# Optimization experiments

Measured on AMD Instinct MI355X. Metric: run time of the kernel, lower is better.

Reference implementation:

```python
import jax, jax.numpy as jnp
import numpy as np

NUM_HEADS = 8
EMBED_DIM = 512
EXPAND = 3
RPE_DIM = 512
RPE_LAYERS = 3
B, N = 4, 2048
D1 = (EXPAND * EMBED_DIM) // NUM_HEADS * NUM_HEADS  # 1536
HEAD_DIM = D1 // NUM_HEADS  # 192


def srms(x):
    # SimpleRMSNorm: x / (||x||_2 * d^{-1/2} + eps)
    d = x.shape[-1]
    rms = jnp.linalg.norm(x, axis=-1, keepdims=True) * (d ** -0.5)
    return x / (rms + 1e-8)


def rpe_net(idx, Wp, bp, Wl, bl, Wr, br):
    # idx: (m, 1) relative positions -> (m, h*head_dim)
    h = idx @ Wp.T + bp
    for i in range(Wl.shape[0]):  # fixed small layer count
        h = jax.nn.relu(srms(h)) @ Wl[i].T + bl[i]
    return jax.nn.relu(srms(h)) @ Wr.T + br


def setup_inputs() -> dict:
    key = jax.random.key(0)
    ks = jax.random.split(key, 12)
    s = 0.02
    return {
        "x": jax.random.normal(ks[0], (B, N, EMBED_DIM), jnp.float32),
        "Wu": jax.random.normal(ks[1], (D1, EMBED_DIM), jnp.float32) * s,
        "bu": jnp.zeros((D1,), jnp.float32),
        "Wv": jax.random.normal(ks[2], (D1, EMBED_DIM), jnp.float32) * s,
        "bv": jnp.zeros((D1,), jnp.float32),
        "Wo": jax.random.normal(ks[3], (EMBED_DIM, D1), jnp.float32) * s,
        "bo": jnp.zeros((EMBED_DIM,), jnp.float32),
        "Wp": jax.random.normal(ks[4], (RPE_DIM, 1), jnp.float32) * s,
        "bp": jax.random.normal(ks[5], (RPE_DIM,), jnp.float32) * s,
        "Wl": jax.random.normal(ks[6], (RPE_LAYERS, RPE_DIM, RPE_DIM), jnp.float32) * s,
        "bl": jax.random.normal(ks[7], (RPE_LAYERS, RPE_DIM), jnp.float32) * s,
        "Wr": jax.random.normal(ks[8], (NUM_HEADS * HEAD_DIM, RPE_DIM), jnp.float32) * s,
        "br": jax.random.normal(ks[9], (NUM_HEADS * HEAD_DIM,), jnp.float32) * s,
    }


def reference(x, Wu, bu, Wv, bv, Wo, bo, Wp, bp, Wl, bl, Wr, br):
    b, n, e = x.shape
    d1 = Wu.shape[0]
    hd = d1 // NUM_HEADS
    u = jax.nn.silu(x @ Wu.T + bu)                       # (b, n, d1)
    v = jax.nn.silu(x @ Wv.T + bv)                       # (b, n, d1)
    v = v.reshape(b, n, NUM_HEADS, hd).transpose(0, 2, 1, 3)  # (b, h, n, d)
    # Tno non-causal, par_type=1: indices [0, 1..n-1, 0, -(n-1)..-1]
    pos = jnp.arange(1, n, dtype=x.dtype)
    zero = jnp.zeros((1,), x.dtype)
    idx = jnp.concatenate([zero, pos, zero, -pos[::-1]])[:, None]  # (2n, 1)
    a = rpe_net(idx, Wp, bp, Wl, bl, Wr, br)             # (2n, h*d)
    a = a.reshape(2 * n, NUM_HEADS, hd).transpose(1, 0, 2)  # (h, 2n, d)
    m = 2 * n
    # circular conv of length 2n along sequence, truncate to n
    y = jnp.fft.rfft(v, m, axis=2) * jnp.fft.rfft(a, m, axis=1)[None]
    out = jnp.fft.irfft(y, m, axis=2)[:, :, :n, :]       # (b, h, n, d)
    out = out.transpose(0, 2, 1, 3).reshape(b, n, d1)    # (b, n, d1)
    return (u * out) @ Wo.T + bo
```

## Files before the change

kernel.cpp:

```cpp
#include <hip/hip_runtime.h>

#define N_SEQ 2048
#define M_FFT 4096
#define D1    1536
#define NH    8
#define HD    192
#define ED    512

typedef __bf16 bf16;
typedef __bf16 bf16x4 __attribute__((ext_vector_type(4)));
typedef __bf16 bf16x8 __attribute__((ext_vector_type(8)));
typedef float  floatx4 __attribute__((ext_vector_type(4)));
typedef float  cx __attribute__((ext_vector_type(2)));

enum { MODE_PLAIN = 0, MODE_SILU_UV = 1, MODE_AT = 3, MODE_RPE = 4 };

__device__ __forceinline__ void gload16(const void* g, void* l) {
    __builtin_amdgcn_global_load_lds(
        (const __attribute__((address_space(1))) void*)g,
        (__attribute__((address_space(3))) void*)l, 16, 0, 0);
}

template<int MODE, typename OutT>
__global__ __launch_bounds__(256) void gemm_bf16(
    const bf16* __restrict__ A, const bf16* __restrict__ Bw,
    const float* __restrict__ bias, const float* __restrict__ bias2,
    OutT* __restrict__ C, OutT* __restrict__ C2,
    int M, int Nc, int K,
    const float* __restrict__ scale_in, float* __restrict__ sumsq_out)
{
    __shared__ __align__(16) bf16 As[2][128 * 32];
    __shared__ __align__(16) bf16 Bs[2][128 * 32];

    const int tid  = threadIdx.x;
    const int row0 = blockIdx.y * 128;
    const int col0 = blockIdx.x * 128;
    const int wid  = tid >> 6;
    const int lane = tid & 63;
    const int lm   = lane & 15;
    const int lk   = lane >> 4;
    const int wm   = wid >> 1;
    const int wn   = wid & 1;
    const int ldrow  = tid >> 2;
    const int ldcol8 = (tid & 3) * 8;

    floatx4 acc[4][4] = {};

    const bf16* Ag = A  + ((size_t)(row0 + ldrow)) * K + ldcol8;
    const bf16* Bg = Bw + ((size_t)(col0 + ldrow)) * K + ldcol8;
    const int woff = (wid * 16) * 32;

    auto stage = [&](int k0, int buf) {
        gload16(Ag + k0, &As[buf][woff]);
        gload16(Ag + (size_t)64 * K + k0, &As[buf][woff + 64 * 32]);
        gload16(Bg + k0, &Bs[buf][woff]);
        gload16(Bg + (size_t)64 * K + k0, &Bs[buf][woff + 64 * 32]);
    };
    auto compute = [&](int buf) {
        bf16x8 af[4], bfr[4];
        #pragma unroll
        for (int mi = 0; mi < 4; ++mi)
            af[mi] = *(const bf16x8*)&As[buf][(wm * 64 + mi * 16 + lm) * 32 + lk * 8];
        #pragma unroll
        for (int nj = 0; nj < 4; ++nj)
            bfr[nj] = *(const bf16x8*)&Bs[buf][(wn * 64 + nj * 16 + lm) * 32 + lk * 8];
        #pragma unroll
        for (int mi = 0; mi < 4; ++mi)
            #pragma unroll
            for (int nj = 0; nj < 4; ++nj)
                acc[mi][nj] = __builtin_amdgcn_mfma_f32_16x16x32_bf16(
                    af[mi], bfr[nj], acc[mi][nj], 0, 0, 0);
    };

    const int nt = K >> 5;
    stage(0, 0);
    __syncthreads();
    for (int t = 0; t < nt; t += 2) {
        stage((t + 1) << 5, 1);
        compute(0);
        __syncthreads();
        if (t + 2 < nt) stage((t + 2) << 5, 0);
        compute(1);
        __syncthreads();
    }

    const float* bs = bias;
    OutT* dst = C;
    int cadj = 0;
    if (MODE == MODE_SILU_UV && col0 >= D1) { bs = bias2; dst = C2; cadj = D1; }

    float bcol[4];
    #pragma unroll
    for (int nj = 0; nj < 4; ++nj)
        bcol[nj] = bs[col0 - cadj + wn * 64 + nj * 16 + lm];

    if (MODE == MODE_RPE) {
        #pragma unroll
        for (int mi = 0; mi < 4; ++mi) {
            #pragma unroll
            for (int r = 0; r < 4; ++r) {
                const int row = row0 + wm * 64 + mi * 16 + lk * 4 + r;
                float sc = 1.0f;
                if (scale_in)
                    sc = 1.0f / (sqrtf(scale_in[row]) * 0.04419417382415922f + 1e-8f);
                float ssq = 0.0f;
                #pragma unroll
                for (int nj = 0; nj < 4; ++nj) {
                    const int col = col0 + wn * 64 + nj * 16 + lm;
                    float val = acc[mi][nj][r] * sc + bcol[nj];
                    ssq += val * val;
                    ((bf16*)C)[(size_t)row * Nc + col] = (bf16)fmaxf(val, 0.0f);
                }
                ssq += __shfl_xor(ssq, 1, 64);
                ssq += __shfl_xor(ssq, 2, 64);
                ssq += __shfl_xor(ssq, 4, 64);
                ssq += __shfl_xor(ssq, 8, 64);
                if (lm == 0) atomicAdd(&sumsq_out[row], ssq);
            }
        }
        return;
    }

    #pragma unroll
    for (int mi = 0; mi < 4; ++mi) {
        const int rbase = row0 + wm * 64 + mi * 16 + lk * 4;
        float sc[4];
        #pragma unroll
        for (int r = 0; r < 4; ++r) {
            sc[r] = 1.0f;
            if (MODE == MODE_AT && scale_in)
                sc[r] = 1.0f / (sqrtf(scale_in[rbase + r]) * 0.04419417382415922f + 1e-8f);
        }
        #pragma unroll
        for (int nj = 0; nj < 4; ++nj) {
            const int col = col0 - cadj + wn * 64 + nj * 16 + lm;
            float vals[4];
            #pragma unroll
            for (int r = 0; r < 4; ++r) {
                float val = acc[mi][nj][r] * sc[r] + bcol[nj];
                if (MODE == MODE_SILU_UV)
                    val = val / (1.0f + __expf(-val));
                vals[r] = val;
            }
            if (MODE == MODE_SILU_UV) {
                int b = rbase >> 11, s = rbase & 2047;
                bf16x4 o;
                #pragma unroll
                for (int r = 0; r < 4; ++r) o[r] = (bf16)vals[r];
                *(bf16x4*)&((bf16*)dst)[((size_t)(b * D1 + col)) * N_SEQ + s] = o;
            } else if (MODE == MODE_AT) {
                float4 o = make_float4(vals[0], vals[1], vals[2], vals[3]);
                *(float4*)&((float*)C)[(size_t)col * M + rbase] = o;
            } else {
                #pragma unroll
                for (int r = 0; r < 4; ++r)
                    C[(size_t)(rbase + r) * Nc + col] = (OutT)vals[r];
            }
        }
    }
}

__global__ __launch_bounds__(256) void f2b_all_kernel(
    const float* __restrict__ x,  const float* __restrict__ s0,
    const float* __restrict__ s1, const float* __restrict__ s2,
    const float* __restrict__ s3, const float* __restrict__ s4,
    const float* __restrict__ Wp, const float* __restrict__ bp,
    bf16* __restrict__ x_bf, bf16* __restrict__ w_bf,
    float* __restrict__ sumsq, bf16* __restrict__ g0,
    float* __restrict__ twd)
{
    const int bid = blockIdx.x;
    const int tid = threadIdx.x;
    __shared__ float red[4];

    if (bid < 7936) {
        const float* src;
        bf16* dst;
        size_t off;
        if (bid < 4096) {
            src = x; dst = x_bf; off = (size_t)bid * 1024;
        } else {
            int t = bid - 4096;
            int seg = t / 768;
            src = seg == 0 ? s0 : seg == 1 ? s1 : seg == 2 ? s2
                : seg == 3 ? s3 : s4;
            dst = w_bf + (size_t)seg * 786432;
            off = (size_t)(t % 768) * 1024;
        }
        size_t i = off + (size_t)tid * 4;
        float4 f = *(const float4*)(src + i);
        union { bf16 h[4]; short4 s; } u4;
        u4.h[0] = (bf16)f.x; u4.h[1] = (bf16)f.y;
        u4.h[2] = (bf16)f.z; u4.h[3] = (bf16)f.w;
        *(short4*)(dst + i) = u4.s;
    } else if (bid < 7948) {
        size_t i = (size_t)(bid - 7936) * 1024 + (size_t)tid * 4;
        *(float4*)(sumsq + i) = make_float4(0.f, 0.f, 0.f, 0.f);
    } else if (bid < 12044) {
        const int j = bid - 7948;
        float idxv = (j < N_SEQ) ? (float)j
                                 : (j == N_SEQ ? 0.0f : (float)(j - 2 * N_SEQ));
        float h1 = idxv * Wp[tid] + bp[tid];
        float h2 = idxv * Wp[tid + 256] + bp[tid + 256];
        float ss = h1 * h1 + h2 * h2;
        #pragma unroll
        for (int off = 32; off > 0; off >>= 1) ss += __shfl_down(ss, off, 64);
        if ((tid & 63) == 0) red[tid >> 6] = ss;
        __syncthreads();
        float tot = red[0] + red[1] + red[2] + red[3];
        float scale = 1.0f / (sqrtf(tot) * 0.04419417382415922f + 1e-8f);
        g0[(size_t)j * ED + tid]       = (bf16)fmaxf(h1 * scale, 0.0f);
        g0[(size_t)j * ED + tid + 256] = (bf16)fmaxf(h2 * scale, 0.0f);
    } else {
        const int idx = (bid - 12044) * 256 + tid;
        const int j = idx >> 4, tau = idx & 15;
        float sA, cA;
        __sincosf(-6.283185307179586f * (float)(j * tau) * (1.0f / 4096.0f),
                  &sA, &cA);
        cx w; w.x = cA; w.y = sA;
        ((cx*)twd)[idx] = w;
    }
}

#define FFT_LDS_SZ 4381

__device__ __forceinline__ int fpad(int i) { return i + (i >> 4) + 2 * (i >> 8); }

__device__ __forceinline__ cx mkcx(float a, float b) { cx r; r.x = a; r.y = b; return r; }
__device__ __forceinline__ cx cmul(cx a, cx b) {
    cx br = mkcx(-b.y, b.x);
    return a.xx * b + a.yy * br;
}
__device__ __forceinline__ cx cmul_cj(cx a, cx b) {
    cx bc = mkcx(b.x, -b.y);
    cx br = mkcx(b.y, b.x);
    return a.xx * bc + a.yy * br;
}
__device__ __forceinline__ cx cneg_i(cx a) { return mkcx(a.y, -a.x); }
__device__ __forceinline__ cx cpos_i(cx a) { return mkcx(-a.y, a.x); }
__host__ __device__ constexpr int brev4(int t) {
    return ((t & 1) << 3) | ((t & 2) << 1) | ((t & 4) >> 1) | ((t & 8) >> 3);
}

#define CC1 0.9238795325112867f
#define SS1 0.3826834323650898f
#define RR2 0.7071067811865476f

template<bool HZ>
__device__ __forceinline__ void fft16_dif_r4(cx x[16]) {
    const cx W1 = mkcx( CC1, -SS1);
    const cx W2 = mkcx( RR2, -RR2);
    const cx W3 = mkcx( SS1, -CC1);
    const cx W6 = mkcx(-RR2, -RR2);
    const cx W9 = mkcx(-CC1,  SS1);
    #pragma unroll
    for (int n = 0; n < 4; ++n) {
        cx A, B, C, D;
        if (HZ) { A = x[n]; C = x[n]; B = x[n + 4]; D = x[n + 4]; }
        else {
            A = x[n] + x[n + 8];      C = x[n] - x[n + 8];
            B = x[n + 4] + x[n + 12]; D = x[n + 4] - x[n + 12];
        }
        cx s = A - B;
        cx nid = cneg_i(D);
        cx m = C + nid;
        cx p = C - nid;
        x[n] = A + B;
        if (n == 0)      { x[4] = s;            x[8]  = m;           x[12] = p; }
        else if (n == 1) { x[5] = cmul(s, W2);  x[9]  = cmul(m, W1); x[13] = cmul(p, W3); }
        else if (n == 2) { x[6] = cneg_i(s);    x[10] = cmul(m, W2); x[14] = cmul(p, W6); }
        else             { x[7] = cmul(s, W6);  x[11] = cmul(m, W3); x[15] = cmul(p, W9); }
    }
    #pragma unroll
    for (int q = 0; q < 16; q += 4) {
        cx a = x[q], b = x[q + 1], c = x[q + 2], d = x[q + 3];
        cx a1 = a + c, c1 = a - c;
        cx b1 = b + d, d1 = cneg_i(b - d);
        x[q]     = a1 + b1;
        x[q + 1] = a1 - b1;
        x[q + 2] = c1 + d1;
        x[q + 3] = c1 - d1;
    }
}

template<bool HALF_OUT>
__device__ __forceinline__ void fft16_dit_inv_r4(cx x[16]) {
    const cx V1 = mkcx( CC1, SS1);
    const cx V2 = mkcx( RR2, RR2);
    const cx V3 = mkcx( SS1, CC1);
    const cx V6 = mkcx(-RR2, RR2);
    #pragma unroll
    for (int q = 0; q < 16; q += 4) {
        cx a = x[q], b = x[q + 1], c = x[q + 2], d = x[q + 3];
        cx a1 = a + b, b1 = a - b;
        cx c1 = c + d, d1 = c - d;
        cx t = cpos_i(d1);
        x[q]     = a1 + c1;
        x[q + 2] = a1 - c1;
        x[q + 1] = b1 + t;
        x[q + 3] = b1 - t;
    }
    #pragma unroll
    for (int n = 0; n < 4; ++n) {
        cx t1, t2;
        if (n == 0)      { t1 = x[4];             t2 = x[12]; }
        else if (n == 1) { t1 = cmul(x[5],  V2);  t2 = cmul(x[13], V2); }
        else if (n == 2) { t1 = cpos_i(x[6]);     t2 = cpos_i(x[14]); }
        else             { t1 = cmul(x[7],  V6);  t2 = cmul(x[15], V6); }
        cx P = x[n] + t1, Q = x[n] - t1;
        cx R = x[n + 8] + t2, S = x[n + 8] - t2;
        cx t, u;
        if (n == 0)      { t = R;            u = S; }
        else if (n == 1) { t = cmul(R, V1);  u = cmul(S, V1); }
        else if (n == 2) { t = cmul(R, V2);  u = cmul(S, V2); }
        else             { t = cmul(R, V3);  u = cmul(S, V3); }
        cx iu = cpos_i(u);
        x[n]     = P + t;
        x[n + 4] = Q + iu;
        if (!HALF_OUT) {
            x[n + 8]  = P - t;
            x[n + 12] = Q - iu;
        }
    }
}

template<bool CONJ>
__device__ __forceinline__ void apply_tw(cx v[16], const cx tw[16]) {
    #pragma unroll
    for (int tau = 1; tau < 16; ++tau) {
        const int q = brev4(tau);
        v[q] = CONJ ? cmul_cj(v[q], tw[tau]) : cmul(v[q], tw[tau]);
    }
}

template<bool CONJ>
__device__ __forceinline__ void apply_tw_lds(cx v[16], const cx* twrow) {
    #pragma unroll
    for (int tau = 1; tau < 16; ++tau) {
        cx w = twrow[tau * 16];
        const int q = brev4(tau);
        v[q] = CONJ ? cmul_cj(v[q], w) : cmul(v[q], w);
    }
}

__device__ __forceinline__ void fwd_s1_store_hz(
    const cx vin[8], const cx tw[16], cx* d, int tid)
{
    cx x[16];
    #pragma unroll
    for (int t = 0; t < 8; ++t) x[t] = vin[t];
    fft16_dif_r4<true>(x);
    apply_tw<false>(x, tw);
    cx* base = d + fpad(tid);
    #pragma unroll
    for (int p = 0; p < 16; ++p) base[274 * p] = x[p];
}

__device__ __forceinline__ void fwd_s2(cx* d, int tid, const cx* tw2lds)
{
    cx v[16];
    cx* base = d + fpad(((tid >> 4) << 8) + (tid & 15));
    #pragma unroll
    for (int t = 0; t < 16; ++t) v[t] = base[17 * t];
    fft16_dif_r4<false>(v);
    apply_tw_lds<false>(v, tw2lds + (tid & 15));
    #pragma unroll
    for (int p = 0; p < 16; ++p) base[17 * p] = v[p];
}

__device__ __forceinline__ void fwd_s3(cx* d, int tid)
{
    cx v[16];
    cx* base = d + fpad(tid << 4);
    #pragma unroll
    for (int t = 0; t < 16; ++t) v[t] = base[t];
    fft16_dif_r4<false>(v);
    #pragma unroll
    for (int p = 0; p < 16; ++p) base[p] = v[p];
}

__device__ __forceinline__ void inv_s2(cx* d, int tid, const cx* tw2lds)
{
    cx v[16];
    cx* base = d + fpad(((tid >> 4) << 8) + (tid & 15));
    #pragma unroll
    for (int p = 0; p < 16; ++p) v[p] = base[17 * p];
    apply_tw_lds<true>(v, tw2lds + (tid & 15));
    fft16_dit_inv_r4<false>(v);
    #pragma unroll
    for (int t = 0; t < 16; ++t) base[17 * t] = v[t];
}

__device__ __forceinline__ void inv_s3_half(cx* d, int tid, const cx tw[16])
{
    cx v[16];
    cx* base = d + fpad(tid);
    #pragma unroll
    for (int p = 0; p < 16; ++p) v[p] = base[274 * p];
    apply_tw<true>(v, tw);
    fft16_dit_inv_r4<true>(v);
    #pragma unroll
    for (int t = 0; t < 8; ++t) base[274 * t] = v[t];
}

__device__ __forceinline__ void pointwise_read(
    const cx* d, int tid, const float4 a0pf[8], const float4 a1pf[8],
    cx v[16])
{
    auto pf = [](const float4* p, int i) -> cx {
        return (i & 1) ? mkcx(p[i >> 1].z, p[i >> 1].w)
                       : mkcx(p[i >> 1].x, p[i >> 1].y);
    };
    const int pbase = tid << 4;
    if (tid == 0) {
        #pragma unroll
        for (int i = 0; i < 16; ++i) {
            const int p2 = (i < 2) ? i : (i ^ ((1 << (31 - __clz(i))) - 1));
            cx Zk = d[fpad(i)];
            cx Zm = d[fpad(p2)];
            cx cjZm = mkcx(Zm.x, -Zm.y);
            cx V0 = Zk + cjZm;
            cx V1 = cneg_i(Zk - cjZm);
            v[i] = cmul(V0, pf(a0pf, i)) + cpos_i(cmul(V1, pf(a1pf, i)));
        }
    } else {
        const int mask = (1 << (31 - __clz(pbase))) - 1;
        const cx* zb  = d + fpad(pbase);
        const cx* zb2 = d + fpad((pbase ^ mask) - 15);
        #pragma unroll
        for (int i = 0; i < 16; ++i) {
            cx Zk = zb[i];
            cx Zm = zb2[15 - i];
            cx cjZm = mkcx(Zm.x, -Zm.y);
            cx V0 = Zk + cjZm;
            cx V1 = cneg_i(Zk - cjZm);
            v[i] = cmul(V0, pf(a0pf, i)) + cpos_i(cmul(V1, pf(a1pf, i)));
        }
    }
}

template<bool HALF_ZERO>
__device__ __forceinline__ void fft4096_fwd_core(
    cx* d, int tid, const cx tw[16], const cx* tw2lds, cx v[16])
{
    {
        fft16_dif_r4<HALF_ZERO>(v);
        apply_tw<false>(v, tw);
        cx* base = d + fpad(tid);
        #pragma unroll
        for (int p = 0; p < 16; ++p) base[274 * p] = v[p];
    }
    __syncthreads();
    fwd_s2(d, tid, tw2lds);
    __syncthreads();
    fwd_s3(d, tid);
    __syncthreads();
}

__global__ __launch_bounds__(256, 4) void fft_a_kernel(
    const float* a_t, cx* __restrict__ A0s, cx* A1s,
    const cx* __restrict__ Twd)
{
    __shared__ cx data[FFT_LDS_SZ];
    __shared__ cx tw2lds[256];
    const int tid = threadIdx.x;
    const int r = blockIdx.x;

    cx tw[16];
    {
        const cx* Tr1 = Twd + (tid << 4);
        #pragma unroll
        for (int t = 1; t < 16; ++t) tw[t] = Tr1[t];
        tw2lds[(tid >> 4) * 16 + (tid & 15)] = Twd[(tid & 15) * 256 + (tid >> 4)];
    }

    const float* r0 = a_t + (size_t)(2 * r) * M_FFT;
    const float* r1 = r0 + M_FFT;
    cx v[16];
    #pragma unroll
    for (int t = 0; t < 16; ++t)
        v[t] = mkcx(r0[tid + 256 * t], r1[tid + 256 * t]);

    fft4096_fwd_core<false>(data, tid, tw, tw2lds, v);

    const float c = 0.25f / 4096.0f;
    cx* A0row = A0s + (size_t)r * 4096;
    cx* A1row = A1s + (size_t)r * 4096;
    if (tid == 0) {
        #pragma unroll
        for (int i = 0; i < 16; ++i) {
            const int p2 = (i < 2) ? i : (i ^ ((1 << (31 - __clz(i))) - 1));
            cx Wk = data[fpad(i)];
            cx Wm = data[fpad(p2)];
            cx cjWm = mkcx(Wm.x, -Wm.y);
            A0row[i] = c * (Wk + cjWm);
            A1row[i] = c * cneg_i(Wk - cjWm);
        }
    } else {
        const int base = tid << 4;
        const int mask = (1 << (31 - __clz(base))) - 1;
        const cx* zb  = data + fpad(base);
        const cx* zb2 = data + fpad((base ^ mask) - 15);
        #pragma unroll
        for (int i = 0; i < 16; ++i) {
            cx Wk = zb[i];
            cx Wm = zb2[15 - i];
            cx cjWm = mkcx(Wm.x, -Wm.y);
            A0row[base + i] = c * (Wk + cjWm);
            A1row[base + i] = c * cneg_i(Wk - cjWm);
        }
    }
}

__global__ __launch_bounds__(256, 2) void fft_conv_kernel(
    const bf16* __restrict__ v_t, const cx* __restrict__ A0s,
    const cx* __restrict__ A1s, const bf16* __restrict__ u_t,
    bf16* __restrict__ gated_t, const cx* __restrict__ Twd)
{
    __shared__ cx data[2][FFT_LDS_SZ];
    __shared__ cx tw2lds[256];
    const int tid = threadIdx.x;
    const int bx = blockIdx.x;
    const int xcd  = bx & 7;
    const int slot = bx >> 3;
    const int bp   = slot & 1;
    const int r    = (slot >> 1) * 8 + xcd;
    const int ch   = 2 * r;
    const int b0   = 2 * bp;
    const int b1   = 2 * bp + 1;

    cx tw[16];
    {
        const cx* Tr1 = Twd + (tid << 4);
        #pragma unroll
        for (int t = 1; t < 16; ++t) tw[t] = Tr1[t];
        tw2lds[(tid >> 4) * 16 + (tid & 15)] = Twd[(tid & 15) * 256 + (tid >> 4)];
    }

    const bf16* z00 = v_t + ((size_t)(b0 * D1 + ch)) * N_SEQ;
    const bf16* z01 = z00 + N_SEQ;
    const bf16* z10 = v_t + ((size_t)(b1 * D1 + ch)) * N_SEQ;
    const bf16* z11 = z10 + N_SEQ;
    {
        cx w0[8], w1[8];
        #pragma unroll
        for (int t = 0; t < 8; ++t)
            w0[t] = mkcx((float)z00[tid + 256 * t], (float)z01[tid + 256 * t]);
        #pragma unroll
        for (int t = 0; t < 8; ++t)
            w1[t] = mkcx((float)z10[tid + 256 * t], (float)z11[tid + 256 * t]);
        fwd_s1_store_hz(w0, tw, data[0], tid);
        fwd_s1_store_hz(w1, tw, data[1], tid);
    }
    __syncthreads();

    fwd_s2(data[0], tid, tw2lds);
    fwd_s2(data[1], tid, tw2lds);
    __syncthreads();

    const int pbase = tid << 4;
    float4 a0pf[8], a1pf[8];
    {
        const float4* A0p = (const float4*)(A0s + (size_t)r * 4096 + pbase);
        const float4* A1p = (const float4*)(A1s + (size_t)r * 4096 + pbase);
        #pragma unroll
        for (int i = 0; i < 8; ++i) { a0pf[i] = A0p[i]; a1pf[i] = A1p[i]; }
    }
    fwd_s3(data[0], tid);
    fwd_s3(data[1], tid);
    __syncthreads();

    cx vA[16], vB[16];
    pointwise_read(data[0], tid, a0pf, a1pf, vA);
    pointwise_read(data[1], tid, a0pf, a1pf, vB);
    __syncthreads();
    fft16_dit_inv_r4<false>(vA);
    fft16_dit_inv_r4<false>(vB);
    {
        cx* baseA = data[0] + fpad(pbase);
        cx* baseB = data[1] + fpad(pbase);
        #pragma unroll
        for (int i = 0; i < 16; ++i) baseA[i] = vA[i];
        #pragma unroll
        for (int i = 0; i < 16; ++i) baseB[i] = vB[i];
    }
    __syncthreads();

    const bf16* u00 = u_t + ((size_t)(b0 * D1 + ch)) * N_SEQ;
    const bf16* u01 = u00 + N_SEQ;
    const bf16* u10 = u_t + ((size_t)(b1 * D1 + ch)) * N_SEQ;
    const bf16* u11 = u10 + N_SEQ;
    bf16x8 ua0 = *(const bf16x8*)(u00 + tid * 8);
    bf16x8 ub0 = *(const bf16x8*)(u01 + tid * 8);
    bf16x8 ua1 = *(const bf16x8*)(u10 + tid * 8);
    bf16x8 ub1 = *(const bf16x8*)(u11 + tid * 8);

    inv_s2(data[0], tid, tw2lds);
    inv_s2(data[1], tid, tw2lds);
    __syncthreads();

    inv_s3_half(data[0], tid, tw);
    inv_s3_half(data[1], tid, tw);
    __syncthreads();

    {
        const int t = tid * 8;
        bf16* g00 = gated_t + ((size_t)(b0 * D1 + ch)) * N_SEQ;
        bf16* g01 = g00 + N_SEQ;
        bf16* g10 = gated_t + ((size_t)(b1 * D1 + ch)) * N_SEQ;
        bf16* g11 = g10 + N_SEQ;
        const cx* baseA = data[0] + fpad(t);
        const cx* baseB = data[1] + fpad(t);
        bf16x8 oa, ob, oc, od;
        #pragma unroll
        for (int i = 0; i < 8; ++i) {
            cx ya = baseA[i];
            cx yb = baseB[i];
            oa[i] = (bf16)(ya.x * (float)ua0[i]);
            ob[i] = (bf16)(ya.y * (float)ub0[i]);
            oc[i] = (bf16)(yb.x * (float)ua1[i]);
            od[i] = (bf16)(yb.y * (float)ub1[i]);
        }
        *(bf16x8*)(g00 + t) = oa;
        *(bf16x8*)(g01 + t) = ob;
        *(bf16x8*)(g10 + t) = oc;
        *(bf16x8*)(g11 + t) = od;
    }
}

__global__ __launch_bounds__(256) void transpose_cs_kernel(
    const bf16* __restrict__ in, bf16* __restrict__ outp)
{
    __shared__ bf16 tile[64 * 68];
    const int c0 = blockIdx.x * 64;
    const int m0 = blockIdx.y * 64;
    const int b  = m0 >> 11;
    const int s0 = m0 & 2047;
    const int tid = threadIdx.x;
    const int cl = tid >> 4;
    const int sc = (tid & 15) * 4;
    #pragma unroll
    for (int p = 0; p < 4; ++p) {
        int c = p * 16 + cl;
        bf16x4 v = *(const bf16x4*)&in[((size_t)(b * D1 + c0 + c)) * N_SEQ + s0 + sc];
        *(bf16x4*)&tile[c * 68 + sc] = v;
    }
    __syncthreads();
    const int sl = tid >> 4;
    const int cc = (tid & 15) * 4;
    #pragma unroll
    for (int p = 0; p < 4; ++p) {
        int s = p * 16 + sl;
        bf16x4 o;
        #pragma unroll
        for (int j = 0; j < 4; ++j) o[j] = tile[(cc + j) * 68 + s];
        *(bf16x4*)&outp[((size_t)(m0 + s)) * D1 + c0 + cc] = o;
    }
}

extern "C" void kernel_launch(void* const* d_in, const int* in_sizes, int n_in,
                              void* d_out, int out_size, void* d_ws, size_t ws_size,
                              hipStream_t stream)
{
    const float* x  = (const float*)d_in[0];
    const float* Wu = (const float*)d_in[1];
    const float* bu = (const float*)d_in[2];
    const float* Wv = (const float*)d_in[3];
    const float* bv = (const float*)d_in[4];
    const float* Wo = (const float*)d_in[5];
    const float* bo = (const float*)d_in[6];
    const float* Wp = (const float*)d_in[7];
    const float* bp = (const float*)d_in[8];
    const float* Wl = (const float*)d_in[9];
    const float* bl = (const float*)d_in[10];
    const float* Wr = (const float*)d_in[11];
    const float* br = (const float*)d_in[12];
    float* out = (float*)d_out;

    float* ws      = (float*)d_ws;
    float* a_t     = ws;
    float* A0spec  = a_t   + 6291456;
    float* sumsq   = A0spec + 6291456;
    float* twd     = sumsq + 12288;
    bf16*  bfws    = (bf16*)(twd + 8192);
    bf16*  x_bf    = bfws;
    bf16*  w_bf    = x_bf    + 4194304;
    bf16*  Wuv_bf  = w_bf;
    bf16*  Wo_bf   = w_bf    + 2 * 786432;
    bf16*  Wl_bf   = Wo_bf   + 786432;
    bf16*  Wr_bf   = Wl_bf   + 786432;
    bf16*  gA      = Wr_bf   + 786432;
    bf16*  gB      = gA      + 2097152;
    bf16*  u_t     = gB      + 2097152;
    bf16*  v_t     = u_t     + 12582912;
    bf16*  gated_t = v_t     + 12582912;
    bf16*  gated   = gated_t + 12582912;

    dim3 blk(256);

    f2b_all_kernel<<<4096 + 5 * 768 + 12 + 4096 + 16, blk, 0, stream>>>(
        x, Wu, Wv, Wo, Wl, Wr, Wp, bp, x_bf, w_bf, sumsq, gA, twd);

    gemm_bf16<MODE_SILU_UV, bf16><<<dim3(24, 64), blk, 0, stream>>>(
        x_bf, Wuv_bf, bu, bv, u_t, v_t, 8192, 2 * D1, ED, nullptr, nullptr);

    bf16* gin = gA;
    bf16* gout = gB;
    for (int i = 0; i < 3; ++i) {
        const float* sin_p = (i == 0) ? nullptr : sumsq + (size_t)(i - 1) * 4096;
        gemm_bf16<MODE_RPE, bf16><<<dim3(4, 32), blk, 0, stream>>>(
            gin, Wl_bf + (size_t)i * ED * ED, bl + (size_t)i * ED, nullptr,
            gout, nullptr, 4096, ED, ED, sin_p, sumsq + (size_t)i * 4096);
        bf16* t = gin; gin = gout; gout = t;
    }
    gemm_bf16<MODE_AT, float><<<dim3(12, 32), blk, 0, stream>>>(
        gin, Wr_bf, br, nullptr, a_t, nullptr, 4096, D1, ED,
        sumsq + 2 * 4096, nullptr);

    fft_a_kernel<<<768, blk, 0, stream>>>(
        a_t, (cx*)A0spec, (cx*)a_t, (const cx*)twd);
    fft_conv_kernel<<<1536, blk, 0, stream>>>(
        v_t, (const cx*)A0spec, (const cx*)a_t, u_t, gated_t, (const cx*)twd);

    transpose_cs_kernel<<<dim3(24, 128), blk, 0, stream>>>(gated_t, gated);

    gemm_bf16<MODE_PLAIN, float><<<dim3(4, 64), blk, 0, stream>>>(
        gated, Wo_bf, bo, nullptr, out, nullptr, 8192, ED, D1,
        nullptr, nullptr);
}
```

Measured before the change: 352.4 us.

## Deepen GEMM LDS pipeline to four stages with explicit vmcnt waits

Replaces the double-buffered GEMM main loop with a 4-buffer ring that keeps three K-tiles of global-to-LDS loads in flight. Explicit s_waitcnt vmcnt counts and raw s_barrier calls replace __syncthreads so compute on one tile overlaps the loads of later tiles. Also switches the SiLU divide to a fast reciprocal. The larger buffers double LDS use per block, which may lower occupancy, and the tail assumes K/32 is a multiple of 4 and at least 4.

```diff
diff --git a/kernel.cpp b/kernel.cpp
--- a/kernel.cpp
+++ b/kernel.cpp
@@ -29,8 +29,8 @@
     int M, int Nc, int K,
     const float* __restrict__ scale_in, float* __restrict__ sumsq_out)
 {
-    __shared__ __align__(16) bf16 As[2][128 * 32];
-    __shared__ __align__(16) bf16 Bs[2][128 * 32];
+    __shared__ __align__(16) bf16 As[4][128 * 32];
+    __shared__ __align__(16) bf16 Bs[4][128 * 32];
 
     const int tid  = threadIdx.x;
     const int row0 = blockIdx.y * 128;
@@ -50,7 +50,8 @@
     const bf16* Bg = Bw + ((size_t)(col0 + ldrow)) * K + ldcol8;
     const int woff = (wid * 16) * 32;
 
-    auto stage = [&](int k0, int buf) {
+    auto stage = [&](int t, int buf) {
+        const int k0 = t << 5;
         gload16(Ag + k0, &As[buf][woff]);
         gload16(Ag + (size_t)64 * K + k0, &As[buf][woff + 64 * 32]);
         gload16(Bg + k0, &Bs[buf][woff]);
@@ -72,17 +73,32 @@
                     af[mi], bfr[nj], acc[mi][nj], 0, 0, 0);
     };
 
+#define GEMM_STEP(T, BUF, DOSTAGE, VM)                                  \
+    do {                                                                \
+        __builtin_amdgcn_s_barrier();          \
+        __builtin_amdgcn_sched_barrier(0);                              \
+        if (DOSTAGE) stage((T) + 3, ((T) + 3) & 3);                     \
+        asm volatile("s_waitcnt vmcnt(" #VM ")" ::: "memory");          \
+        __builtin_amdgcn_s_barrier();          \
+        __builtin_amdgcn_sched_barrier(0);                              \
+        compute(BUF);                                                   \
+    } while (0)
+
     const int nt = K >> 5;
     stage(0, 0);
-    __syncthreads();
-    for (int t = 0; t < nt; t += 2) {
-        stage((t + 1) << 5, 1);
-        compute(0);
-        __syncthreads();
-        if (t + 2 < nt) stage((t + 2) << 5, 0);
-        compute(1);
-        __syncthreads();
-    }
+    stage(1, 1);
+    stage(2, 2);
+    for (int t4 = 0; t4 < nt - 4; t4 += 4) {
+        GEMM_STEP(t4 + 0, 0, true, 12);
+        GEMM_STEP(t4 + 1, 1, true, 12);
+        GEMM_STEP(t4 + 2, 2, true, 12);
+        GEMM_STEP(t4 + 3, 3, true, 12);
+    }
+    GEMM_STEP(nt - 4, 0, true, 12);
+    GEMM_STEP(nt - 3, 1, false, 8);
+    GEMM_STEP(nt - 2, 2, false, 4);
+    GEMM_STEP(nt - 1, 3, false, 0);
+#undef GEMM_STEP
 
     const float* bs = bias;
     OutT* dst = C;
@@ -139,7 +155,7 @@
             for (int r = 0; r < 4; ++r) {
                 float val = acc[mi][nj][r] * sc[r] + bcol[nj];
                 if (MODE == MODE_SILU_UV)
-                    val = val / (1.0f + __expf(-val));
+                    val = val * __fdividef(1.0f, 1.0f + __expf(-val));
                 vals[r] = val;
             }
             if (MODE == MODE_SILU_UV) {
```

After: 341.9 us. -3.0%, faster.
